# Performance work log

Hardware: AMD Instinct MI355X
Metric: run time of the kernel (lower is better)

The kernel has to match this reference:

```python
import jax, jax.numpy as jnp
import numpy as np

T, H, I, E, K, L, R = 1024, 2048, 1024, 16, 2, 4, 16


def setup_inputs() -> dict:
    key = jax.random.key(0)
    ks = jax.random.split(key, 10)
    hidden_states = jax.random.normal(ks[0], (T, H), jnp.float32)
    topk_ids = jax.random.randint(ks[1], (T, K), 0, E, dtype=jnp.int32)
    topk_weights = jax.random.uniform(ks[2], (T, K), jnp.float32)
    lora_indices = jax.random.randint(ks[3], (T,), 0, L, dtype=jnp.int32)
    lora_ranks = jax.random.randint(ks[4], (L,), 1, R + 1, dtype=jnp.int32)
    scalings = jax.random.uniform(ks[5], (L,), jnp.float32) + 0.5
    w1 = jax.random.normal(ks[6], (E, 2 * I, H), jnp.float32) * 0.02  # fused gate+up
    w2 = jax.random.normal(ks[7], (E, H, I), jnp.float32) * 0.02      # down proj
    lora_a = jax.random.normal(ks[8], (L, E, R, H), jnp.float32) * 0.02
    lora_b = jax.random.normal(ks[9], (L, E, H, R), jnp.float32) * 0.02
    return dict(hidden_states=hidden_states, topk_ids=topk_ids, topk_weights=topk_weights,
                lora_indices=lora_indices, lora_ranks=lora_ranks, scalings=scalings,
                w1=w1, w2=w2, lora_a=lora_a, lora_b=lora_b)


def reference(hidden_states, topk_ids, topk_weights, lora_indices, lora_ranks, scalings,
              w1, w2, lora_a, lora_b):
    x = hidden_states  # [T, H]
    # ---- Base FusedMoE (SiLU-gated), dense over all experts then routed ----
    h1 = jnp.einsum('th,efh->tef', x, w1)                 # [T, E, 2I]
    gate, up = jnp.split(h1, 2, axis=-1)                  # [T, E, I] each
    act = jax.nn.silu(gate) * up                          # [T, E, I]
    expert_out = jnp.einsum('tei,ehi->teh', act, w2)      # [T, E, H]
    route = jnp.zeros((T, E), x.dtype).at[jnp.arange(T)[:, None], topk_ids].add(topk_weights)
    base = jnp.einsum('te,teh->th', route, expert_out)    # [T, H]
    # ---- Per-expert LoRA delta (moe_dispatch + grouped LoRA GEMM) ----
    l_pair = jnp.broadcast_to(lora_indices[:, None], (T, K)).reshape(-1)  # [P], P=T*K
    e_pair = topk_ids.reshape(-1)                                         # [P]
    valid = l_pair >= 0
    l_safe = jnp.maximum(l_pair, 0)
    flat_idx = l_safe * E + e_pair                                        # index into [L*E, ...]
    A = jnp.take(lora_a.reshape(L * E, R, H), flat_idx, axis=0)           # [P, R, H]
    B = jnp.take(lora_b.reshape(L * E, H, R), flat_idx, axis=0)           # [P, H, R]
    xp = jnp.repeat(x, K, axis=0)                                         # [P, H]
    a = jnp.einsum('ph,prh->pr', xp, A)                                   # [P, R]
    ranks = jnp.maximum(lora_ranks, 1)
    rmask = jnp.arange(R)[None, :] < ranks[l_safe][:, None]               # variable rank mask
    a = jnp.where(rmask, a, 0.0) * scalings[l_safe][:, None]
    delta = jnp.einsum('pr,phr->ph', a, B)                                # [P, H]
    delta = jnp.where(valid[:, None], delta, 0.0)
    delta = delta.reshape(T, K, H).sum(axis=1)                            # merge (token,k) pairs
    return base + delta
```

## Files before the change

kernel.cpp:

```cpp
#include <hip/hip_runtime.h>
#include <math.h>

constexpr int T = 1024;
constexpr int H = 2048;
constexpr int I = 1024;
constexpr int E = 16;
constexpr int K = 2;
constexpr int L = 4;
constexpr int R = 16;
constexpr int P = T * K;
constexpr int MT_MAX = 32;

typedef __attribute__((ext_vector_type(8))) short bf16x8;
typedef __attribute__((ext_vector_type(4))) float f32x4;

__device__ inline unsigned short f2bf(float f) {
  unsigned u = __builtin_bit_cast(unsigned, f);
  u = (u + 0x7FFFu + ((u >> 16) & 1u)) >> 16;
  return (unsigned short)u;
}

__device__ inline bf16x8 pack8(f32x4 a, f32x4 b) {
  bf16x8 v;
  v[0] = (short)f2bf(a[0]); v[1] = (short)f2bf(a[1]);
  v[2] = (short)f2bf(a[2]); v[3] = (short)f2bf(a[3]);
  v[4] = (short)f2bf(b[0]); v[5] = (short)f2bf(b[1]);
  v[6] = (short)f2bf(b[2]); v[7] = (short)f2bf(b[3]);
  return v;
}

__device__ inline void st8(unsigned short* s, int r, int c, bf16x8 v) {
  int byte = ((r << 6) + c) * 2;
  byte ^= (r & 7) << 4;
  *reinterpret_cast<bf16x8*>(reinterpret_cast<char*>(s) + byte) = v;
}
__device__ inline bf16x8 ld8(const unsigned short* s, int r, int c) {
  int byte = ((r << 6) + c) * 2;
  byte ^= (r & 7) << 4;
  return *reinterpret_cast<const bf16x8*>(reinterpret_cast<const char*>(s) + byte);
}

__global__ __launch_bounds__(256) void route_kernel(
    const int* __restrict__ topk_ids, const float* __restrict__ topk_w,
    int* __restrict__ eoff, int* __restrict__ pair_t,
    float* __restrict__ pair_w, int* __restrict__ pair_e,
    int* __restrict__ tile_e, int* __restrict__ tile_m0, int* __restrict__ ntiles) {
  __shared__ int cnt[E];
  __shared__ int off[E + 1];
  __shared__ int cur[E];
  const int tid = threadIdx.x;
  if (tid < E) cnt[tid] = 0;
  __syncthreads();
  for (int p = tid; p < P; p += blockDim.x) atomicAdd(&cnt[topk_ids[p]], 1);
  __syncthreads();
  if (tid == 0) {
    off[0] = 0;
    for (int e = 0; e < E; ++e) off[e + 1] = off[e] + cnt[e];
    int nt = 0;
    for (int e = 0; e < E; ++e)
      for (int m0 = 0; m0 < cnt[e]; m0 += 128) {
        tile_e[nt] = e;
        tile_m0[nt] = m0;
        ++nt;
      }
    *ntiles = nt;
  }
  __syncthreads();
  if (tid < E) cur[tid] = off[tid];
  if (tid <= E) eoff[tid] = off[tid];
  __syncthreads();
  for (int p = tid; p < P; p += blockDim.x) {
    const int e = topk_ids[p];
    const int pos = atomicAdd(&cur[e], 1);
    pair_t[pos] = p / K;
    pair_w[pos] = topk_w[p];
    pair_e[pos] = e;
  }
}

__global__ __launch_bounds__(256) void xcvt_zero(const float* __restrict__ x,
                                                unsigned short* __restrict__ xb,
                                                float* __restrict__ out) {
  const int i = (blockIdx.x * 256 + threadIdx.x) * 8;
  f32x4 a = *reinterpret_cast<const f32x4*>(x + i);
  f32x4 b = *reinterpret_cast<const f32x4*>(x + i + 4);
  *reinterpret_cast<bf16x8*>(xb + i) = pack8(a, b);
  const f32x4 z = {0.f, 0.f, 0.f, 0.f};
  *reinterpret_cast<f32x4*>(out + i) = z;
  *reinterpret_cast<f32x4*>(out + i + 4) = z;
}

__global__ __launch_bounds__(256) void gemm1_mfma(
    const unsigned short* __restrict__ xb, const float* __restrict__ w1,
    const int* __restrict__ eoff, const int* __restrict__ pair_t,
    const int* __restrict__ tile_e, const int* __restrict__ tile_m0,
    const int* __restrict__ ntiles, unsigned short* __restrict__ act) {
  const int bid = blockIdx.x;
  const int mt = bid >> 4;
  if (mt >= *ntiles) return;
  const int it = bid & 15;
  const int e = tile_e[mt];
  const int m0 = tile_m0[mt];
  const int beg = eoff[e];
  const int cnt = eoff[e + 1] - beg;
  const int i0 = it * 64;

  __shared__ unsigned short sX[128 * 64];
  __shared__ unsigned short sG[64 * 64];
  __shared__ unsigned short sU[64 * 64];

  const int tid = threadIdx.x;
  const int xr = tid >> 1, xc = (tid & 1) * 32;
  const int gr = tid >> 2, gc = (tid & 3) * 16;

  const int rm = m0 + xr;
  const int tok = (rm < cnt) ? pair_t[beg + rm] : -1;
  const unsigned short* xrow = xb + (size_t)(tok < 0 ? 0 : tok) * H + xc;
  const float* grow = w1 + ((size_t)e * (2 * I) + i0 + gr) * H + gc;
  const float* urow = grow + (size_t)I * H;

  const int lane = tid & 63, wid = tid >> 6;
  const int wm = wid << 5;
  const int fr = lane & 15, fq = lane >> 4;

  f32x4 ag[2][4], au[2][4];
#pragma unroll
  for (int a = 0; a < 2; ++a)
#pragma unroll
    for (int b = 0; b < 4; ++b) {
      ag[a][b] = {0.f, 0.f, 0.f, 0.f};
      au[a][b] = {0.f, 0.f, 0.f, 0.f};
    }

  bf16x8 rx[4];
  f32x4 rg[4], ru[4];
  const bf16x8 zero8 = {0, 0, 0, 0, 0, 0, 0, 0};

  auto LOAD = [&](int kk) {
    if (tok >= 0) {
#pragma unroll
      for (int s = 0; s < 4; ++s)
        rx[s] = *reinterpret_cast<const bf16x8*>(xrow + kk + s * 8);
    } else {
#pragma unroll
      for (int s = 0; s < 4; ++s) rx[s] = zero8;
    }
#pragma unroll
    for (int s = 0; s < 4; ++s) {
      rg[s] = *reinterpret_cast<const f32x4*>(grow + kk + s * 4);
      ru[s] = *reinterpret_cast<const f32x4*>(urow + kk + s * 4);
    }
  };

  constexpr int NT = H / 64;
  LOAD(0);
  for (int t = 0; t < NT; ++t) {
    const bf16x8 wg0 = pack8(rg[0], rg[1]), wg1 = pack8(rg[2], rg[3]);
    const bf16x8 wu0 = pack8(ru[0], ru[1]), wu1 = pack8(ru[2], ru[3]);
    __syncthreads();
    st8(sX, xr, xc + 0, rx[0]); st8(sX, xr, xc + 8, rx[1]);
    st8(sX, xr, xc + 16, rx[2]); st8(sX, xr, xc + 24, rx[3]);
    st8(sG, gr, gc, wg0); st8(sG, gr, gc + 8, wg1);
    st8(sU, gr, gc, wu0); st8(sU, gr, gc + 8, wu1);
    if (t + 1 < NT) LOAD((t + 1) * 64);
    __syncthreads();
#pragma unroll
    for (int kb = 0; kb < 2; ++kb) {
      const int k8 = (kb << 5) + (fq << 3);
      bf16x8 af[2], gf[4], uf[4];
#pragma unroll
      for (int mi = 0; mi < 2; ++mi) af[mi] = ld8(sX, wm + (mi << 4) + fr, k8);
#pragma unroll
      for (int nj = 0; nj < 4; ++nj) {
        gf[nj] = ld8(sG, (nj << 4) + fr, k8);
        uf[nj] = ld8(sU, (nj << 4) + fr, k8);
      }
#pragma unroll
      for (int mi = 0; mi < 2; ++mi)
#pragma unroll
        for (int nj = 0; nj < 4; ++nj) {
          ag[mi][nj] = __builtin_amdgcn_mfma_f32_16x16x32_bf16(af[mi], gf[nj], ag[mi][nj], 0, 0, 0);
          au[mi][nj] = __builtin_amdgcn_mfma_f32_16x16x32_bf16(af[mi], uf[nj], au[mi][nj], 0, 0, 0);
        }
    }
  }

#pragma unroll
  for (int mi = 0; mi < 2; ++mi)
#pragma unroll
    for (int q = 0; q < 4; ++q) {
      const int m = m0 + wm + (mi << 4) + (fq << 2) + q;
      if (m >= cnt) continue;
#pragma unroll
      for (int nj = 0; nj < 4; ++nj) {
        const float g = ag[mi][nj][q];
        const float u = au[mi][nj][q];
        const float s = g / (1.f + __expf(-g));
        act[(size_t)(beg + m) * I + i0 + (nj << 4) + fr] = f2bf(s * u);
      }
    }
}

__global__ __launch_bounds__(256) void gemm2_mfma(
    const unsigned short* __restrict__ act, const float* __restrict__ w2,
    const int* __restrict__ eoff, const int* __restrict__ pair_t,
    const float* __restrict__ pair_w, const int* __restrict__ tile_e,
    const int* __restrict__ tile_m0, const int* __restrict__ ntiles,
    float* __restrict__ out) {
  const int bid = blockIdx.x;
  const int mt = bid >> 5;
  if (mt >= *ntiles) return;
  const int ht = bid & 31;
  const int e = tile_e[mt];
  const int m0 = tile_m0[mt];
  const int beg = eoff[e];
  const int cnt = eoff[e + 1] - beg;
  const int h0 = ht * 64;

  __shared__ unsigned short sA[128 * 64];
  __shared__ unsigned short sB[64 * 64];

  const int tid = threadIdx.x;
  const int ar = tid >> 1, ac = (tid & 1) * 32;
  const int br = tid >> 2, bc = (tid & 3) * 16;

  const bool av = (m0 + ar) < cnt;
  const unsigned short* arow = act + (size_t)(beg + (av ? m0 + ar : 0)) * I + ac;
  const float* brow = w2 + ((size_t)e * H + h0 + br) * I + bc;

  const int lane = tid & 63, wid = tid >> 6;
  const int wm = wid << 5;
  const int fr = lane & 15, fq = lane >> 4;

  f32x4 acc[2][4];
#pragma unroll
  for (int a = 0; a < 2; ++a)
#pragma unroll
    for (int b = 0; b < 4; ++b) acc[a][b] = {0.f, 0.f, 0.f, 0.f};

  bf16x8 ra[4];
  f32x4 rb[4];

  auto LOAD = [&](int kk) {
#pragma unroll
    for (int s = 0; s < 4; ++s) {
      ra[s] = *reinterpret_cast<const bf16x8*>(arow + kk + s * 8);
      rb[s] = *reinterpret_cast<const f32x4*>(brow + kk + s * 4);
    }
  };

  constexpr int NT = I / 64;
  LOAD(0);
  for (int t = 0; t < NT; ++t) {
    const bf16x8 wb0 = pack8(rb[0], rb[1]), wb1 = pack8(rb[2], rb[3]);
    __syncthreads();
    st8(sA, ar, ac + 0, ra[0]); st8(sA, ar, ac + 8, ra[1]);
    st8(sA, ar, ac + 16, ra[2]); st8(sA, ar, ac + 24, ra[3]);
    st8(sB, br, bc, wb0); st8(sB, br, bc + 8, wb1);
    if (t + 1 < NT) LOAD((t + 1) * 64);
    __syncthreads();
#pragma unroll
    for (int kb = 0; kb < 2; ++kb) {
      const int k8 = (kb << 5) + (fq << 3);
      bf16x8 af[2], bf[4];
#pragma unroll
      for (int mi = 0; mi < 2; ++mi) af[mi] = ld8(sA, wm + (mi << 4) + fr, k8);
#pragma unroll
      for (int nj = 0; nj < 4; ++nj) bf[nj] = ld8(sB, (nj << 4) + fr, k8);
#pragma unroll
      for (int mi = 0; mi < 2; ++mi)
#pragma unroll
        for (int nj = 0; nj < 4; ++nj)
          acc[mi][nj] = __builtin_amdgcn_mfma_f32_16x16x32_bf16(af[mi], bf[nj], acc[mi][nj], 0, 0, 0);
    }
  }

#pragma unroll
  for (int mi = 0; mi < 2; ++mi)
#pragma unroll
    for (int q = 0; q < 4; ++q) {
      const int m = m0 + wm + (mi << 4) + (fq << 2) + q;
      if (m >= cnt) continue;
      const int tt = pair_t[beg + m];
      const float w = pair_w[beg + m];
#pragma unroll
      for (int nj = 0; nj < 4; ++nj)
        atomicAdd(out + (size_t)tt * H + h0 + (nj << 4) + fr, w * acc[mi][nj][q]);
    }
}

__global__ __launch_bounds__(256) void lora_kernel(
    const float* __restrict__ x, const float* __restrict__ lora_a,
    const float* __restrict__ lora_b, const int* __restrict__ lora_idx,
    const int* __restrict__ lora_ranks, const float* __restrict__ scalings,
    const int* __restrict__ pair_t, const int* __restrict__ pair_e,
    float* __restrict__ out) {
  const int p = blockIdx.x;
  const int t = pair_t[p];
  const int e = pair_e[p];
  const int l = lora_idx[t];
  if (l < 0) return;
  int rank = lora_ranks[l];
  if (rank < 1) rank = 1;
  const float sc = scalings[l];

  __shared__ float a_sh[R];
  const int tid = threadIdx.x;
  const int wave = tid >> 6, lane = tid & 63;
  const float4* xv = reinterpret_cast<const float4*>(x + (size_t)t * H);
  const float* Ab = lora_a + (size_t)(l * E + e) * R * H;
#pragma unroll
  for (int q = 0; q < 4; ++q) {
    const int r = (wave << 2) | q;
    const float4* Av = reinterpret_cast<const float4*>(Ab + (size_t)r * H);
    float s = 0.f;
#pragma unroll
    for (int it = 0; it < H / 256; ++it) {
      const int h4 = it * 64 + lane;
      const float4 xx = xv[h4];
      const float4 aa = Av[h4];
      s += xx.x * aa.x + xx.y * aa.y + xx.z * aa.z + xx.w * aa.w;
    }
#pragma unroll
    for (int off = 32; off; off >>= 1) s += __shfl_xor(s, off);
    if (lane == 0) a_sh[r] = (r < rank) ? s * sc : 0.f;
  }
  __syncthreads();
  const float* Bb = lora_b + (size_t)(l * E + e) * H * R;
  for (int h = tid; h < H; h += 256) {
    const float4* Bv = reinterpret_cast<const float4*>(Bb + (size_t)h * R);
    float d = 0.f;
#pragma unroll
    for (int r4 = 0; r4 < 4; ++r4) {
      const float4 bb = Bv[r4];
      d += a_sh[r4 * 4 + 0] * bb.x + a_sh[r4 * 4 + 1] * bb.y +
           a_sh[r4 * 4 + 2] * bb.z + a_sh[r4 * 4 + 3] * bb.w;
    }
    atomicAdd(out + (size_t)t * H + h, d);
  }
}

extern "C" void kernel_launch(void* const* d_in, const int* in_sizes, int n_in,
                              void* d_out, int out_size, void* d_ws, size_t ws_size,
                              hipStream_t stream) {
  const float* x          = (const float*)d_in[0];
  const int*   topk_ids   = (const int*)d_in[1];
  const float* topk_w     = (const float*)d_in[2];
  const int*   lora_idx   = (const int*)d_in[3];
  const int*   lora_ranks = (const int*)d_in[4];
  const float* scalings   = (const float*)d_in[5];
  const float* w1         = (const float*)d_in[6];
  const float* w2         = (const float*)d_in[7];
  const float* lora_a     = (const float*)d_in[8];
  const float* lora_b     = (const float*)d_in[9];
  float* out = (float*)d_out;

  char* ws = (char*)d_ws;
  int*   eoff    = (int*)(ws);
  int*   ntiles  = (int*)(ws + 96);
  int*   tile_e  = (int*)(ws + 256);
  int*   tile_m0 = (int*)(ws + 384);
  int*   pair_t  = (int*)(ws + 512);
  int*   pair_e  = (int*)(ws + 512 + 4 * P);
  float* pair_w  = (float*)(ws + 512 + 8 * P);
  unsigned short* xb  = (unsigned short*)(ws + 32768);
  unsigned short* act = (unsigned short*)(ws + 32768 + (size_t)T * H * 2);

  xcvt_zero<<<T * H / (256 * 8), 256, 0, stream>>>(x, xb, out);
  route_kernel<<<1, 256, 0, stream>>>(topk_ids, topk_w, eoff, pair_t, pair_w, pair_e,
                                      tile_e, tile_m0, ntiles);
  gemm1_mfma<<<MT_MAX * 16, 256, 0, stream>>>(xb, w1, eoff, pair_t, tile_e, tile_m0,
                                              ntiles, act);
  gemm2_mfma<<<MT_MAX * 32, 256, 0, stream>>>(act, w2, eoff, pair_t, pair_w, tile_e,
                                              tile_m0, ntiles, out);
  lora_kernel<<<P, 256, 0, stream>>>(x, lora_a, lora_b, lora_idx, lora_ranks, scalings,
                                     pair_t, pair_e, out);
}
```

Before: 208.2 us.

## Merge prep kernels, fuse LoRA into gemm1 launch, halve GEMM N-tiles

```diff
diff --git a/kernel.cpp b/kernel.cpp
--- a/kernel.cpp
+++ b/kernel.cpp
@@ -10,6 +10,9 @@
 constexpr int R = 16;
 constexpr int P = T * K;
 constexpr int MT_MAX = 32;
+constexpr int G_CVT = T * H / (256 * 8);
+constexpr int G1 = MT_MAX * 32;
+constexpr int G2 = MT_MAX * 64;
 
 typedef __attribute__((ext_vector_type(8))) short bf16x8;
 typedef __attribute__((ext_vector_type(4))) float f32x4;
@@ -40,18 +43,30 @@
   return *reinterpret_cast<const bf16x8*>(reinterpret_cast<const char*>(s) + byte);
 }
 
-__global__ __launch_bounds__(256) void route_kernel(
+__global__ __launch_bounds__(256) void prep_kernel(
+    const float* __restrict__ x, unsigned short* __restrict__ xb,
+    float* __restrict__ out,
     const int* __restrict__ topk_ids, const float* __restrict__ topk_w,
     int* __restrict__ eoff, int* __restrict__ pair_t,
     float* __restrict__ pair_w, int* __restrict__ pair_e,
     int* __restrict__ tile_e, int* __restrict__ tile_m0, int* __restrict__ ntiles) {
+  const int tid = threadIdx.x;
+  if (blockIdx.x < G_CVT) {
+    const int i = (blockIdx.x * 256 + tid) * 8;
+    f32x4 a = *reinterpret_cast<const f32x4*>(x + i);
+    f32x4 b = *reinterpret_cast<const f32x4*>(x + i + 4);
+    *reinterpret_cast<bf16x8*>(xb + i) = pack8(a, b);
+    const f32x4 z = {0.f, 0.f, 0.f, 0.f};
+    *reinterpret_cast<f32x4*>(out + i) = z;
+    *reinterpret_cast<f32x4*>(out + i + 4) = z;
+    return;
+  }
   __shared__ int cnt[E];
   __shared__ int off[E + 1];
   __shared__ int cur[E];
-  const int tid = threadIdx.x;
   if (tid < E) cnt[tid] = 0;
   __syncthreads();
-  for (int p = tid; p < P; p += blockDim.x) atomicAdd(&cnt[topk_ids[p]], 1);
+  for (int p = tid; p < P; p += 256) atomicAdd(&cnt[topk_ids[p]], 1);
   __syncthreads();
   if (tid == 0) {
     off[0] = 0;
@@ -69,7 +84,7 @@
   if (tid < E) cur[tid] = off[tid];
   if (tid <= E) eoff[tid] = off[tid];
   __syncthreads();
-  for (int p = tid; p < P; p += blockDim.x) {
+  for (int p = tid; p < P; p += 256) {
     const int e = topk_ids[p];
     const int pos = atomicAdd(&cur[e], 1);
     pair_t[pos] = p / K;
@@ -78,127 +93,167 @@
   }
 }
 
-__global__ __launch_bounds__(256) void xcvt_zero(const float* __restrict__ x,
-                                                unsigned short* __restrict__ xb,
-                                                float* __restrict__ out) {
-  const int i = (blockIdx.x * 256 + threadIdx.x) * 8;
-  f32x4 a = *reinterpret_cast<const f32x4*>(x + i);
-  f32x4 b = *reinterpret_cast<const f32x4*>(x + i + 4);
-  *reinterpret_cast<bf16x8*>(xb + i) = pack8(a, b);
-  const f32x4 z = {0.f, 0.f, 0.f, 0.f};
-  *reinterpret_cast<f32x4*>(out + i) = z;
-  *reinterpret_cast<f32x4*>(out + i + 4) = z;
-}
-
-__global__ __launch_bounds__(256) void gemm1_mfma(
+__global__ __launch_bounds__(256) void gemm1_lora(
     const unsigned short* __restrict__ xb, const float* __restrict__ w1,
     const int* __restrict__ eoff, const int* __restrict__ pair_t,
     const int* __restrict__ tile_e, const int* __restrict__ tile_m0,
-    const int* __restrict__ ntiles, unsigned short* __restrict__ act) {
-  const int bid = blockIdx.x;
-  const int mt = bid >> 4;
-  if (mt >= *ntiles) return;
-  const int it = bid & 15;
-  const int e = tile_e[mt];
-  const int m0 = tile_m0[mt];
-  const int beg = eoff[e];
-  const int cnt = eoff[e + 1] - beg;
-  const int i0 = it * 64;
-
-  __shared__ unsigned short sX[128 * 64];
-  __shared__ unsigned short sG[64 * 64];
-  __shared__ unsigned short sU[64 * 64];
-
+    const int* __restrict__ ntiles, unsigned short* __restrict__ act,
+    const float* __restrict__ x, const float* __restrict__ lora_a,
+    const float* __restrict__ lora_b, const int* __restrict__ lora_idx,
+    const int* __restrict__ lora_ranks, const float* __restrict__ scalings,
+    const int* __restrict__ pair_e, float* __restrict__ out) {
+  __shared__ __align__(16) char smem[24576];
   const int tid = threadIdx.x;
-  const int xr = tid >> 1, xc = (tid & 1) * 32;
-  const int gr = tid >> 2, gc = (tid & 3) * 16;
-
-  const int rm = m0 + xr;
-  const int tok = (rm < cnt) ? pair_t[beg + rm] : -1;
-  const unsigned short* xrow = xb + (size_t)(tok < 0 ? 0 : tok) * H + xc;
-  const float* grow = w1 + ((size_t)e * (2 * I) + i0 + gr) * H + gc;
-  const float* urow = grow + (size_t)I * H;
-
-  const int lane = tid & 63, wid = tid >> 6;
-  const int wm = wid << 5;
-  const int fr = lane & 15, fq = lane >> 4;
-
-  f32x4 ag[2][4], au[2][4];
-#pragma unroll
-  for (int a = 0; a < 2; ++a)
-#pragma unroll
-    for (int b = 0; b < 4; ++b) {
-      ag[a][b] = {0.f, 0.f, 0.f, 0.f};
-      au[a][b] = {0.f, 0.f, 0.f, 0.f};
-    }
-
-  bf16x8 rx[4];
-  f32x4 rg[4], ru[4];
-  const bf16x8 zero8 = {0, 0, 0, 0, 0, 0, 0, 0};
-
-  auto LOAD = [&](int kk) {
-    if (tok >= 0) {
-#pragma unroll
-      for (int s = 0; s < 4; ++s)
-        rx[s] = *reinterpret_cast<const bf16x8*>(xrow + kk + s * 8);
-    } else {
-#pragma unroll
-      for (int s = 0; s < 4; ++s) rx[s] = zero8;
-    }
-#pragma unroll
-    for (int s = 0; s < 4; ++s) {
-      rg[s] = *reinterpret_cast<const f32x4*>(grow + kk + s * 4);
-      ru[s] = *reinterpret_cast<const f32x4*>(urow + kk + s * 4);
-    }
-  };
-
-  constexpr int NT = H / 64;
-  LOAD(0);
-  for (int t = 0; t < NT; ++t) {
-    const bf16x8 wg0 = pack8(rg[0], rg[1]), wg1 = pack8(rg[2], rg[3]);
-    const bf16x8 wu0 = pack8(ru[0], ru[1]), wu1 = pack8(ru[2], ru[3]);
-    __syncthreads();
-    st8(sX, xr, xc + 0, rx[0]); st8(sX, xr, xc + 8, rx[1]);
-    st8(sX, xr, xc + 16, rx[2]); st8(sX, xr, xc + 24, rx[3]);
-    st8(sG, gr, gc, wg0); st8(sG, gr, gc + 8, wg1);
-    st8(sU, gr, gc, wu0); st8(sU, gr, gc + 8, wu1);
-    if (t + 1 < NT) LOAD((t + 1) * 64);
-    __syncthreads();
-#pragma unroll
-    for (int kb = 0; kb < 2; ++kb) {
-      const int k8 = (kb << 5) + (fq << 3);
-      bf16x8 af[2], gf[4], uf[4];
-#pragma unroll
-      for (int mi = 0; mi < 2; ++mi) af[mi] = ld8(sX, wm + (mi << 4) + fr, k8);
-#pragma unroll
-      for (int nj = 0; nj < 4; ++nj) {
-        gf[nj] = ld8(sG, (nj << 4) + fr, k8);
-        uf[nj] = ld8(sU, (nj << 4) + fr, k8);
-      }
-#pragma unroll
-      for (int mi = 0; mi < 2; ++mi)
-#pragma unroll
-        for (int nj = 0; nj < 4; ++nj) {
-          ag[mi][nj] = __builtin_amdgcn_mfma_f32_16x16x32_bf16(af[mi], gf[nj], ag[mi][nj], 0, 0, 0);
-          au[mi][nj] = __builtin_amdgcn_mfma_f32_16x16x32_bf16(af[mi], uf[nj], au[mi][nj], 0, 0, 0);
+
+  if (blockIdx.x < (unsigned)G1) {
+    const int bid = blockIdx.x;
+    const int mt = bid >> 5;
+    if (mt >= *ntiles) return;
+    const int it = bid & 31;
+    const int e = tile_e[mt];
+    const int m0 = tile_m0[mt];
+    const int beg = eoff[e];
+    const int cnt = eoff[e + 1] - beg;
+    const int i0 = it * 32;
+
+    unsigned short* sX = (unsigned short*)smem;
+    unsigned short* sG = (unsigned short*)(smem + 16384);
+    unsigned short* sU = (unsigned short*)(smem + 20480);
+
+    const int xr = tid >> 1, xc = (tid & 1) * 32;
+    const int gr = tid >> 3, gc = (tid & 7) * 8;
+
+    const int rm = m0 + xr;
+    const int tok = (rm < cnt) ? pair_t[beg + rm] : -1;
+    const unsigned short* xrow = xb + (size_t)(tok < 0 ? 0 : tok) * H + xc;
+    const float* grow = w1 + ((size_t)e * (2 * I) + i0 + gr) * H + gc;
+    const float* urow = grow + (size_t)I * H;
+
+    const int lane = tid & 63, wid = tid >> 6;
+    const int wm = wid << 5;
+    const int fr = lane & 15, fq = lane >> 4;
+
+    f32x4 ag[2][2], au[2][2];
+#pragma unroll
+    for (int a = 0; a < 2; ++a)
+#pragma unroll
+      for (int b = 0; b < 2; ++b) {
+        ag[a][b] = {0.f, 0.f, 0.f, 0.f};
+        au[a][b] = {0.f, 0.f, 0.f, 0.f};
+      }
+
+    bf16x8 rx[4];
+    f32x4 rg[2], ru[2];
+    const bf16x8 zero8 = {0, 0, 0, 0, 0, 0, 0, 0};
+
+    auto LOAD = [&](int kk) {
+      if (tok >= 0) {
+#pragma unroll
+        for (int s = 0; s < 4; ++s)
+          rx[s] = *reinterpret_cast<const bf16x8*>(xrow + kk + s * 8);
+      } else {
+#pragma unroll
+        for (int s = 0; s < 4; ++s) rx[s] = zero8;
+      }
+#pragma unroll
+      for (int s = 0; s < 2; ++s) {
+        rg[s] = *reinterpret_cast<const f32x4*>(grow + kk + s * 4);
+        ru[s] = *reinterpret_cast<const f32x4*>(urow + kk + s * 4);
+      }
+    };
+
+    constexpr int NT = H / 64;
+    LOAD(0);
+    for (int t = 0; t < NT; ++t) {
+      const bf16x8 wg = pack8(rg[0], rg[1]);
+      const bf16x8 wu = pack8(ru[0], ru[1]);
+      __syncthreads();
+      st8(sX, xr, xc + 0, rx[0]); st8(sX, xr, xc + 8, rx[1]);
+      st8(sX, xr, xc + 16, rx[2]); st8(sX, xr, xc + 24, rx[3]);
+      st8(sG, gr, gc, wg);
+      st8(sU, gr, gc, wu);
+      if (t + 1 < NT) LOAD((t + 1) * 64);
+      __syncthreads();
+#pragma unroll
+      for (int kb = 0; kb < 2; ++kb) {
+        const int k8 = (kb << 5) + (fq << 3);
+        bf16x8 af[2], gf[2], uf[2];
+#pragma unroll
+        for (int mi = 0; mi < 2; ++mi) af[mi] = ld8(sX, wm + (mi << 4) + fr, k8);
+#pragma unroll
+        for (int nj = 0; nj < 2; ++nj) {
+          gf[nj] = ld8(sG, (nj << 4) + fr, k8);
+          uf[nj] = ld8(sU, (nj << 4) + fr, k8);
         }
-    }
-  }
-
-#pragma unroll
-  for (int mi = 0; mi < 2; ++mi)
-#pragma unroll
-    for (int q = 0; q < 4; ++q) {
-      const int m = m0 + wm + (mi << 4) + (fq << 2) + q;
-      if (m >= cnt) continue;
-#pragma unroll
-      for (int nj = 0; nj < 4; ++nj) {
-        const float g = ag[mi][nj][q];
-        const float u = au[mi][nj][q];
-        const float s = g / (1.f + __expf(-g));
-        act[(size_t)(beg + m) * I + i0 + (nj << 4) + fr] = f2bf(s * u);
-      }
-    }
+#pragma unroll
+        for (int mi = 0; mi < 2; ++mi)
+#pragma unroll
+          for (int nj = 0; nj < 2; ++nj) {
+            ag[mi][nj] = __builtin_amdgcn_mfma_f32_16x16x32_bf16(af[mi], gf[nj], ag[mi][nj], 0, 0, 0);
+            au[mi][nj] = __builtin_amdgcn_mfma_f32_16x16x32_bf16(af[mi], uf[nj], au[mi][nj], 0, 0, 0);
+          }
+      }
+    }
+
+#pragma unroll
+    for (int mi = 0; mi < 2; ++mi)
+#pragma unroll
+      for (int q = 0; q < 4; ++q) {
+        const int m = m0 + wm + (mi << 4) + (fq << 2) + q;
+        if (m >= cnt) continue;
+#pragma unroll
+        for (int nj = 0; nj < 2; ++nj) {
+          const float g = ag[mi][nj][q];
+          const float u = au[mi][nj][q];
+          const float s = g / (1.f + __expf(-g));
+          act[(size_t)(beg + m) * I + i0 + (nj << 4) + fr] = f2bf(s * u);
+        }
+      }
+    return;
+  }
+
+  const int p = blockIdx.x - G1;
+  const int t = pair_t[p];
+  const int e = pair_e[p];
+  const int l = lora_idx[t];
+  if (l < 0) return;
+  int rank = lora_ranks[l];
+  if (rank < 1) rank = 1;
+  const float sc = scalings[l];
+
+  float* a_sh = (float*)smem;
+  const int wave = tid >> 6, lane = tid & 63;
+  const float4* xv = reinterpret_cast<const float4*>(x + (size_t)t * H);
+  const float* Ab = lora_a + (size_t)(l * E + e) * R * H;
+#pragma unroll
+  for (int q = 0; q < 4; ++q) {
+    const int r = (wave << 2) | q;
+    const float4* Av = reinterpret_cast<const float4*>(Ab + (size_t)r * H);
+    float s = 0.f;
+#pragma unroll
+    for (int it = 0; it < H / 256; ++it) {
+      const int h4 = it * 64 + lane;
+      const float4 xx = xv[h4];
+      const float4 aa = Av[h4];
+      s += xx.x * aa.x + xx.y * aa.y + xx.z * aa.z + xx.w * aa.w;
+    }
+#pragma unroll
+    for (int off = 32; off; off >>= 1) s += __shfl_xor(s, off);
+    if (lane == 0) a_sh[r] = (r < rank) ? s * sc : 0.f;
+  }
+  __syncthreads();
+  const float* Bb = lora_b + (size_t)(l * E + e) * H * R;
+  for (int h = tid; h < H; h += 256) {
+    const float4* Bv = reinterpret_cast<const float4*>(Bb + (size_t)h * R);
+    float d = 0.f;
+#pragma unroll
+    for (int r4 = 0; r4 < 4; ++r4) {
+      const float4 bb = Bv[r4];
+      d += a_sh[r4 * 4 + 0] * bb.x + a_sh[r4 * 4 + 1] * bb.y +
+           a_sh[r4 * 4 + 2] * bb.z + a_sh[r4 * 4 + 3] * bb.w;
+    }
+    atomicAdd(out + (size_t)t * H + h, d);
+  }
 }
 
 __global__ __launch_bounds__(256) void gemm2_mfma(
@@ -208,21 +263,21 @@
     const int* __restrict__ tile_m0, const int* __restrict__ ntiles,
     float* __restrict__ out) {
   const int bid = blockIdx.x;
-  const int mt = bid >> 5;
+  const int mt = bid >> 6;
   if (mt >= *ntiles) return;
-  const int ht = bid & 31;
+  const int ht = bid & 63;
   const int e = tile_e[mt];
   const int m0 = tile_m0[mt];
   const int beg = eoff[e];
   const int cnt = eoff[e + 1] - beg;
-  const int h0 = ht * 64;
+  const int h0 = ht * 32;
 
   __shared__ unsigned short sA[128 * 64];
-  __shared__ unsigned short sB[64 * 64];
+  __shared__ unsigned short sB[32 * 64];
 
   const int tid = threadIdx.x;
   const int ar = tid >> 1, ac = (tid & 1) * 32;
-  const int br = tid >> 2, bc = (tid & 3) * 16;
+  const int br = tid >> 3, bc = (tid & 7) * 8;
 
   const bool av = (m0 + ar) < cnt;
   const unsigned short* arow = act + (size_t)(beg + (av ? m0 + ar : 0)) * I + ac;
@@ -232,45 +287,46 @@
   const int wm = wid << 5;
   const int fr = lane & 15, fq = lane >> 4;
 
-  f32x4 acc[2][4];
+  f32x4 acc[2][2];
 #pragma unroll
   for (int a = 0; a < 2; ++a)
 #pragma unroll
-    for (int b = 0; b < 4; ++b) acc[a][b] = {0.f, 0.f, 0.f, 0.f};
+    for (int b = 0; b < 2; ++b) acc[a][b] = {0.f, 0.f, 0.f, 0.f};
 
   bf16x8 ra[4];
-  f32x4 rb[4];
+  f32x4 rb[2];
 
   auto LOAD = [&](int kk) {
 #pragma unroll
-    for (int s = 0; s < 4; ++s) {
+    for (int s = 0; s < 4; ++s)
       ra[s] = *reinterpret_cast<const bf16x8*>(arow + kk + s * 8);
+#pragma unroll
+    for (int s = 0; s < 2; ++s)
       rb[s] = *reinterpret_cast<const f32x4*>(brow + kk + s * 4);
-    }
   };
 
   constexpr int NT = I / 64;
   LOAD(0);
   for (int t = 0; t < NT; ++t) {
-    const bf16x8 wb0 = pack8(rb[0], rb[1]), wb1 = pack8(rb[2], rb[3]);
+    const bf16x8 wb = pack8(rb[0], rb[1]);
     __syncthreads();
     st8(sA, ar, ac + 0, ra[0]); st8(sA, ar, ac + 8, ra[1]);
     st8(sA, ar, ac + 16, ra[2]); st8(sA, ar, ac + 24, ra[3]);
-    st8(sB, br, bc, wb0); st8(sB, br, bc + 8, wb1);
+    st8(sB, br, bc, wb);
     if (t + 1 < NT) LOAD((t + 1) * 64);
     __syncthreads();
 #pragma unroll
     for (int kb = 0; kb < 2; ++kb) {
       const int k8 = (kb << 5) + (fq << 3);
-      bf16x8 af[2], bf[4];
+      bf16x8 af[2], bf[2];
 #pragma unroll
       for (int mi = 0; mi < 2; ++mi) af[mi] = ld8(sA, wm + (mi << 4) + fr, k8);
 #pragma unroll
-      for (int nj = 0; nj < 4; ++nj) bf[nj] = ld8(sB, (nj << 4) + fr, k8);
+      for (int nj = 0; nj < 2; ++nj) bf[nj] = ld8(sB, (nj << 4) + fr, k8);
 #pragma unroll
       for (int mi = 0; mi < 2; ++mi)
 #pragma unroll
-        for (int nj = 0; nj < 4; ++nj)
+        for (int nj = 0; nj < 2; ++nj)
           acc[mi][nj] = __builtin_amdgcn_mfma_f32_16x16x32_bf16(af[mi], bf[nj], acc[mi][nj], 0, 0, 0);
     }
   }
@@ -284,60 +340,9 @@
       const int tt = pair_t[beg + m];
       const float w = pair_w[beg + m];
 #pragma unroll
-      for (int nj = 0; nj < 4; ++nj)
+      for (int nj = 0; nj < 2; ++nj)
         atomicAdd(out + (size_t)tt * H + h0 + (nj << 4) + fr, w * acc[mi][nj][q]);
     }
-}
-
-__global__ __launch_bounds__(256) void lora_kernel(
-    const float* __restrict__ x, const float* __restrict__ lora_a,
-    const float* __restrict__ lora_b, const int* __restrict__ lora_idx,
-    const int* __restrict__ lora_ranks, const float* __restrict__ scalings,
-    const int* __restrict__ pair_t, const int* __restrict__ pair_e,
-    float* __restrict__ out) {
-  const int p = blockIdx.x;
-  const int t = pair_t[p];
-  const int e = pair_e[p];
-  const int l = lora_idx[t];
-  if (l < 0) return;
-  int rank = lora_ranks[l];
-  if (rank < 1) rank = 1;
-  const float sc = scalings[l];
-
-  __shared__ float a_sh[R];
-  const int tid = threadIdx.x;
-  const int wave = tid >> 6, lane = tid & 63;
-  const float4* xv = reinterpret_cast<const float4*>(x + (size_t)t * H);
-  const float* Ab = lora_a + (size_t)(l * E + e) * R * H;
-#pragma unroll
-  for (int q = 0; q < 4; ++q) {
-    const int r = (wave << 2) | q;
-    const float4* Av = reinterpret_cast<const float4*>(Ab + (size_t)r * H);
-    float s = 0.f;
-#pragma unroll
-    for (int it = 0; it < H / 256; ++it) {
-      const int h4 = it * 64 + lane;
-      const float4 xx = xv[h4];
-      const float4 aa = Av[h4];
-      s += xx.x * aa.x + xx.y * aa.y + xx.z * aa.z + xx.w * aa.w;
-    }
-#pragma unroll
-    for (int off = 32; off; off >>= 1) s += __shfl_xor(s, off);
-    if (lane == 0) a_sh[r] = (r < rank) ? s * sc : 0.f;
-  }
-  __syncthreads();
-  const float* Bb = lora_b + (size_t)(l * E + e) * H * R;
-  for (int h = tid; h < H; h += 256) {
-    const float4* Bv = reinterpret_cast<const float4*>(Bb + (size_t)h * R);
-    float d = 0.f;
-#pragma unroll
-    for (int r4 = 0; r4 < 4; ++r4) {
-      const float4 bb = Bv[r4];
-      d += a_sh[r4 * 4 + 0] * bb.x + a_sh[r4 * 4 + 1] * bb.y +
-           a_sh[r4 * 4 + 2] * bb.z + a_sh[r4 * 4 + 3] * bb.w;
-    }
-    atomicAdd(out + (size_t)t * H + h, d);
-  }
 }
 
 extern "C" void kernel_launch(void* const* d_in, const int* in_sizes, int n_in,
@@ -366,13 +371,11 @@
   unsigned short* xb  = (unsigned short*)(ws + 32768);
   unsigned short* act = (unsigned short*)(ws + 32768 + (size_t)T * H * 2);
 
-  xcvt_zero<<<T * H / (256 * 8), 256, 0, stream>>>(x, xb, out);
-  route_kernel<<<1, 256, 0, stream>>>(topk_ids, topk_w, eoff, pair_t, pair_w, pair_e,
-                                      tile_e, tile_m0, ntiles);
-  gemm1_mfma<<<MT_MAX * 16, 256, 0, stream>>>(xb, w1, eoff, pair_t, tile_e, tile_m0,
-                                              ntiles, act);
-  gemm2_mfma<<<MT_MAX * 32, 256, 0, stream>>>(act, w2, eoff, pair_t, pair_w, tile_e,
-                                              tile_m0, ntiles, out);
-  lora_kernel<<<P, 256, 0, stream>>>(x, lora_a, lora_b, lora_idx, lora_ranks, scalings,
-                                     pair_t, pair_e, out);
-}
+  prep_kernel<<<G_CVT + 1, 256, 0, stream>>>(x, xb, out, topk_ids, topk_w, eoff,
+                                             pair_t, pair_w, pair_e, tile_e, tile_m0, ntiles);
+  gemm1_lora<<<G1 + P, 256, 0, stream>>>(xb, w1, eoff, pair_t, tile_e, tile_m0, ntiles,
+                                         act, x, lora_a, lora_b, lora_idx, lora_ranks,
+                                         scalings, pair_e, out);
+  gemm2_mfma<<<G2, 256, 0, stream>>>(act, w2, eoff, pair_t, pair_w, tile_e, tile_m0,
+                                     ntiles, out);
+}
```

Result: faster. 177.2 us (-14.9%).
